# Optimization experiments

Measured on AMD Instinct MI355X. Metric: run time of the kernel, lower is better.

## Reference

```python
import jax, jax.numpy as jnp
import numpy as np

N_NODES = 50000
N_EDGES = 800000
N_GRAPHS = 128
INPUT_DIM = 64
HIDDEN = 64       # num_heads * dim_per_head = 4 * 16
N_HEADS = 4
DK = HIDDEN // N_HEADS   # 16, per-head key/query dim
DV = HIDDEN // N_HEADS   # 16, per-head value dim
NUM_LAYERS = 4           # -> 3 GIN layers
OUT_DIM = 16
LN_EPS = 1e-5


def layer_norm(x, g, b):
    mu = jnp.mean(x, axis=-1, keepdims=True)
    var = jnp.mean(jnp.square(x - mu), axis=-1, keepdims=True)
    return (x - mu) * jax.lax.rsqrt(var + LN_EPS) * g + b


def sab_block(x, Wq, Wk, Wv, Wo, ln_g, ln_b, add_residual):
    # x: [N, S, D_in]; pre-LN self-attention block (Set Transformer SAB)
    xin = layer_norm(x, ln_g, ln_b)
    q = jnp.einsum('nsd,dhk->nshk', xin, Wq)   # [N,S,H,dk]
    k = jnp.einsum('nsd,dhk->nshk', xin, Wk)
    v = jnp.einsum('nsd,dhk->nshk', xin, Wv)   # [N,S,H,dv]
    scores = jnp.einsum('nqhk,nshk->nhqs', q, k) / jnp.sqrt(jnp.asarray(DK, x.dtype))
    att = jax.nn.softmax(scores, axis=-1)
    o = jnp.einsum('nhqs,nshk->nqhk', att, v)
    o = o.reshape(o.shape[0], o.shape[1], N_HEADS * DV)
    o = o @ Wo                                  # [N,S,dim_out]
    if add_residual:
        o = o + x
    return o


def gin_aggregate(h, src, dst):
    # sum-neighbor aggregation; eps=0, learn_eps=False -> (1+0)*h + sum_nbrs
    msg = jax.ops.segment_sum(h[src], dst, num_segments=N_NODES)
    return h + msg


def setup_inputs() -> dict:
    key = jax.random.key(0)
    ks = jax.random.split(key, 16)
    s = 0.05
    feat = jax.random.normal(ks[0], (N_NODES, 4 * INPUT_DIM), dtype=jnp.float32)
    src = jax.random.randint(ks[1], (N_EDGES,), 0, N_NODES)
    dst = jax.random.randint(ks[2], (N_EDGES,), 0, N_NODES)
    graph_ids = jnp.sort(jax.random.randint(ks[3], (N_NODES,), 0, N_GRAPHS))
    L = NUM_LAYERS - 1  # 3 GIN layers, all same shapes (input_dim == hidden)
    Wq = jax.random.normal(ks[4], (L, HIDDEN, N_HEADS, DK), dtype=jnp.float32) * s
    Wk = jax.random.normal(ks[5], (L, HIDDEN, N_HEADS, DK), dtype=jnp.float32) * s
    Wv = jax.random.normal(ks[6], (L, HIDDEN, N_HEADS, DV), dtype=jnp.float32) * s
    Wo = jax.random.normal(ks[7], (L, N_HEADS * DV, HIDDEN), dtype=jnp.float32) * s
    sab_ln_g = jnp.ones((L, HIDDEN), dtype=jnp.float32)
    sab_ln_b = jnp.zeros((L, HIDDEN), dtype=jnp.float32)
    ln1_g = jnp.ones((L, HIDDEN), dtype=jnp.float32)
    ln1_b = jnp.zeros((L, HIDDEN), dtype=jnp.float32)
    ln2_g = jnp.ones((L, HIDDEN), dtype=jnp.float32)
    ln2_b = jnp.zeros((L, HIDDEN), dtype=jnp.float32)
    W_pred = jax.random.normal(ks[8], (NUM_LAYERS, HIDDEN, OUT_DIM), dtype=jnp.float32) * s
    b_pred = jnp.zeros((NUM_LAYERS, OUT_DIM), dtype=jnp.float32)
    return {"feat": feat, "src": src, "dst": dst, "graph_ids": graph_ids,
            "Wq": Wq, "Wk": Wk, "Wv": Wv, "Wo": Wo,
            "sab_ln_g": sab_ln_g, "sab_ln_b": sab_ln_b,
            "ln1_g": ln1_g, "ln1_b": ln1_b, "ln2_g": ln2_g, "ln2_b": ln2_b,
            "W_pred": W_pred, "b_pred": b_pred}


def reference(feat, src, dst, graph_ids, Wq, Wk, Wv, Wo,
              sab_ln_g, sab_ln_b, ln1_g, ln1_b, ln2_g, ln2_b, W_pred, b_pred):
    h = feat.reshape(N_NODES, -1, INPUT_DIM)   # [N, S, D]
    hidden_rep = [h]
    for i in range(NUM_LAYERS - 1):
        if i == 0:
            agg = gin_aggregate(h, src, dst)
            h = sab_block(agg, Wq[i], Wk[i], Wv[i], Wo[i],
                          sab_ln_g[i], sab_ln_b[i], add_residual=False)
        else:
            h_pre = layer_norm(h, ln1_g[i], ln1_b[i])
            agg = gin_aggregate(h_pre, src, dst)
            h = h + sab_block(agg, Wq[i], Wk[i], Wv[i], Wo[i],
                              sab_ln_g[i], sab_ln_b[i], add_residual=True)
        hidden_rep.append(layer_norm(jax.nn.relu(h), ln2_g[i], ln2_b[i]))
    score = jnp.zeros((N_GRAPHS, hidden_rep[0].shape[1], OUT_DIM), dtype=feat.dtype)
    for i, hh in enumerate(hidden_rep):
        pooled = jax.ops.segment_sum(hh, graph_ids, num_segments=N_GRAPHS)  # [B,S,D]
        score = score + pooled @ W_pred[i] + b_pred[i]
    return score
```

## Files before the change

### kernel.cpp

```cpp
#include <hip/hip_runtime.h>

#define NN 50000
#define NE 800000
#define NG 128
#define RREP 16
#define RSTRIDE 50048

typedef __attribute__((ext_vector_type(8))) short short8;
typedef __attribute__((ext_vector_type(4))) float f32x4;

__device__ __forceinline__ unsigned short f2bf(float f){
  union { float f; unsigned int u; } v; v.f = f;
  return (unsigned short)((v.u + 0x7fffu + ((v.u >> 16) & 1u)) >> 16);
}
__device__ __forceinline__ float bf2f(unsigned short h){
  union { unsigned int u; float f; } v; v.u = ((unsigned int)h) << 16;
  return v.f;
}

__global__ __launch_bounds__(256) void k_goff(const int* __restrict__ gid,
                                              int* __restrict__ goff){
  int i = blockIdx.x*256 + threadIdx.x;
  if (i >= NN) return;
  int c = gid[i];
  int p = (i == 0) ? -1 : gid[i-1];
  for (int g = p+1; g <= c; ++g) goff[g] = i;
  if (i == NN-1){
    for (int g = c+1; g <= NG; ++g) goff[g] = NN;
  }
}

__global__ __launch_bounds__(256) void k_count_rep(const int* __restrict__ idx,
                                                   int* __restrict__ cnt_rep, int n){
  int i = blockIdx.x*256 + threadIdx.x;
  int r = blockIdx.x & (RREP-1);
  if (i < n) atomicAdd(&cnt_rep[r*RSTRIDE + idx[i]], 1);
}

__global__ __launch_bounds__(256) void k_reduce_rep(const int* __restrict__ cnt_rep,
                                                    int* __restrict__ cnt){
  int i = blockIdx.x*256 + threadIdx.x;
  if (i < NN){
    int s = 0;
    #pragma unroll
    for (int r=0; r<RREP; ++r) s += cnt_rep[r*RSTRIDE + i];
    cnt[i] = s;
  }
}

__global__ __launch_bounds__(256) void k_blocksum(const int* __restrict__ in, int n,
                                                  int* __restrict__ bsum){
  __shared__ int ws4[4];
  int i = blockIdx.x*256 + threadIdx.x;
  int v = (i < n) ? in[i] : 0;
  #pragma unroll
  for (int d=1; d<64; d<<=1) v += __shfl_xor(v, d);
  int lane = threadIdx.x & 63, w = threadIdx.x >> 6;
  if (lane == 0) ws4[w] = v;
  __syncthreads();
  if (threadIdx.x == 0) bsum[blockIdx.x] = ws4[0]+ws4[1]+ws4[2]+ws4[3];
}

__global__ __launch_bounds__(256) void k_scan_small(const int* __restrict__ in, int n,
                                                    int* __restrict__ out){
  __shared__ int wsum[4];
  int tid = threadIdx.x, lane = tid & 63, w = tid >> 6;
  int v = (tid < n) ? in[tid] : 0;
  int x = v;
  #pragma unroll
  for (int d=1; d<64; d<<=1){ int y = __shfl_up(x, d); if (lane >= d) x += y; }
  if (lane == 63) wsum[w] = x;
  __syncthreads();
  int pre2 = 0;
  for (int j=0; j<w; ++j) pre2 += wsum[j];
  int incl = x + pre2;
  if (tid < n) out[tid] = incl - v;
  if (tid == n-1) out[n] = incl;
}

__global__ __launch_bounds__(256) void k_scan_apply(const int* __restrict__ in, int n,
                                                    const int* __restrict__ boff,
                                                    int* __restrict__ out){
  __shared__ int wsum[4];
  int tid = threadIdx.x, lane = tid & 63, w = tid >> 6;
  int i = blockIdx.x*256 + tid;
  int v = (i < n) ? in[i] : 0;
  int x = v;
  #pragma unroll
  for (int d=1; d<64; d<<=1){ int y = __shfl_up(x, d); if (lane >= d) x += y; }
  if (lane == 63) wsum[w] = x;
  __syncthreads();
  int pre2 = boff[blockIdx.x];
  for (int j=0; j<w; ++j) pre2 += wsum[j];
  int excl = x - v + pre2;
  if (i < n){
    out[i] = excl;
    if (i == n-1) out[n] = excl + v;
  }
}

__global__ __launch_bounds__(256) void k_fpos_rep(const int* __restrict__ cnt_rep,
                                                  const int* __restrict__ off,
                                                  int* __restrict__ fpos_rep){
  int i = blockIdx.x*256 + threadIdx.x;
  if (i < NN){
    int p = off[i];
    #pragma unroll
    for (int r=0; r<RREP; ++r){
      fpos_rep[r*RSTRIDE + i] = p;
      p += cnt_rep[r*RSTRIDE + i];
    }
  }
}

__global__ __launch_bounds__(256) void k_fill_rep(const int* __restrict__ src,
                                                  const int* __restrict__ dst,
                                                  int* __restrict__ fpos_rep,
                                                  int* __restrict__ csr, int n){
  int i = blockIdx.x*256 + threadIdx.x;
  int r = blockIdx.x & (RREP-1);
  if (i < n){
    int p = atomicAdd(&fpos_rep[r*RSTRIDE + dst[i]], 1);
    csr[p] = src[i];
  }
}

__global__ __launch_bounds__(256) void k_wt(const float* __restrict__ Wq,
                                            const float* __restrict__ Wk,
                                            const float* __restrict__ Wv,
                                            const float* __restrict__ Wo,
                                            unsigned short* __restrict__ Wt){
  int gid = blockIdx.x*256 + threadIdx.x;
  int l   = gid >> 14;
  int rem = gid & 16383;
  int mat = rem >> 12;
  int idx = rem & 4095;
  int c = idx >> 6, n = idx & 63;
  const float* srcp = (mat==0)?Wq:(mat==1)?Wk:(mat==2)?Wv:Wo;
  float v = srcp[l*4096 + idx];
  Wt[l*16384 + (mat*64 + n)*64 + c] = f2bf(v);
}

__global__ __launch_bounds__(256) void k_f2bf(const float* __restrict__ in,
                                              unsigned short* __restrict__ out){
  int i = blockIdx.x*256 + threadIdx.x;
  float4 v = ((const float4*)in)[i];
  ushort4 o; o.x=f2bf(v.x); o.y=f2bf(v.y); o.z=f2bf(v.z); o.w=f2bf(v.w);
  ((ushort4*)out)[i] = o;
}

__global__ __launch_bounds__(256) void k_aggregate(const unsigned short* __restrict__ pre,
                                                   const int* __restrict__ off,
                                                   const int* __restrict__ csr,
                                                   unsigned short* __restrict__ agg){
  int w = threadIdx.x >> 6, lane = threadIdx.x & 63;
  int node = blockIdx.x*4 + w;
  int s = off[node], e = off[node+1];
  const ushort4* base = (const ushort4*)pre;
  ushort4 u = base[node*64 + lane];
  float a0 = bf2f(u.x), a1 = bf2f(u.y), a2 = bf2f(u.z), a3 = bf2f(u.w);
  int i = s;
  for (; i + 4 <= e; i += 4){
    int n0 = csr[i], n1 = csr[i+1], n2 = csr[i+2], n3 = csr[i+3];
    ushort4 u0 = base[n0*64 + lane], u1 = base[n1*64 + lane];
    ushort4 u2 = base[n2*64 + lane], u3 = base[n3*64 + lane];
    a0 += bf2f(u0.x)+bf2f(u1.x)+bf2f(u2.x)+bf2f(u3.x);
    a1 += bf2f(u0.y)+bf2f(u1.y)+bf2f(u2.y)+bf2f(u3.y);
    a2 += bf2f(u0.z)+bf2f(u1.z)+bf2f(u2.z)+bf2f(u3.z);
    a3 += bf2f(u0.w)+bf2f(u1.w)+bf2f(u2.w)+bf2f(u3.w);
  }
  for (; i < e; ++i){
    int n0 = csr[i];
    ushort4 u0 = base[n0*64 + lane];
    a0 += bf2f(u0.x); a1 += bf2f(u0.y); a2 += bf2f(u0.z); a3 += bf2f(u0.w);
  }
  ushort4 o; o.x=f2bf(a0); o.y=f2bf(a1); o.z=f2bf(a2); o.w=f2bf(a3);
  ((ushort4*)agg)[node*64 + lane] = o;
}

__global__ __launch_bounds__(256) void k_sab(unsigned short* __restrict__ agg,
                                             unsigned short* __restrict__ h,
                                             unsigned short* __restrict__ pre_next,
                                             const unsigned short* __restrict__ Wt,
                                             const float* __restrict__ lng,
                                             const float* __restrict__ lnb,
                                             const float* __restrict__ g2,
                                             const float* __restrict__ b2,
                                             const float* __restrict__ g1,
                                             const float* __restrict__ b1,
                                             int residual, int write_pre, int write_h){
  __shared__ unsigned short xo_s[4][16][72];
  __shared__ unsigned short qkv_s[4][16][200];

  int tid = threadIdx.x;
  int w = tid >> 6, lane = tid & 63;
  int c16 = lane & 15, kb = lane >> 4;
  int R0 = blockIdx.x*64 + w*16;

  {
    float4 gv = ((const float4*)lng)[c16];
    float4 bv = ((const float4*)lnb)[c16];
    #pragma unroll
    for (int rr=0; rr<4; ++rr){
      int m = rr*4 + kb;
      ushort4 uv = ((const ushort4*)agg)[(R0+m)*16 + c16];
      float vx = bf2f(uv.x), vy = bf2f(uv.y), vz = bf2f(uv.z), vw = bf2f(uv.w);
      float s = vx+vy+vz+vw;
      float q = vx*vx+vy*vy+vz*vz+vw*vw;
      #pragma unroll
      for (int d=1; d<16; d<<=1){ s += __shfl_xor(s, d); q += __shfl_xor(q, d); }
      float mu = s*(1.f/64.f);
      float rs = rsqrtf(q*(1.f/64.f) - mu*mu + 1e-5f);
      ushort4 o;
      o.x=f2bf((vx-mu)*rs*gv.x+bv.x); o.y=f2bf((vy-mu)*rs*gv.y+bv.y);
      o.z=f2bf((vz-mu)*rs*gv.z+bv.z); o.w=f2bf((vw-mu)*rs*gv.w+bv.w);
      *(ushort4*)&xo_s[w][m][c16*4] = o;
    }
  }

  short8 a0 = *(const short8*)&xo_s[w][c16][kb*8];
  short8 a1 = *(const short8*)&xo_s[w][c16][32 + kb*8];
  f32x4 acc[12];
  #pragma unroll
  for (int t=0; t<12; ++t){
    short8 b0 = *(const short8*)&Wt[(t*16 + c16)*64 + kb*8];
    short8 b1 = *(const short8*)&Wt[(t*16 + c16)*64 + 32 + kb*8];
    f32x4 z = {0.f, 0.f, 0.f, 0.f};
    z = __builtin_amdgcn_mfma_f32_16x16x32_bf16(a0, b0, z, 0, 0, 0);
    z = __builtin_amdgcn_mfma_f32_16x16x32_bf16(a1, b1, z, 0, 0, 0);
    acc[t] = z;
  }
  #pragma unroll
  for (int t=0; t<12; ++t){
    #pragma unroll
    for (int r=0; r<4; ++r)
      qkv_s[w][kb*4 + r][t*16 + c16] = f2bf(acc[t][r]);
  }

  {
    int p = lane >> 2, qr = lane & 3;
    int ns = p >> 2, hd = p & 3;
    int mrow = ns*4 + qr;
    int qc = hd*16, kc = 64 + hd*16, vc = 128 + hd*16;
    float qv[16];
    short8 u0 = *(const short8*)&qkv_s[w][mrow][qc];
    short8 u1 = *(const short8*)&qkv_s[w][mrow][qc+8];
    #pragma unroll
    for (int j=0; j<8; ++j){
      qv[j]   = bf2f((unsigned short)u0[j]);
      qv[8+j] = bf2f((unsigned short)u1[j]);
    }
    float sc[4];
    #pragma unroll
    for (int kr=0; kr<4; ++kr){
      short8 k0 = *(const short8*)&qkv_s[w][ns*4+kr][kc];
      short8 k1 = *(const short8*)&qkv_s[w][ns*4+kr][kc+8];
      float d2 = 0.f;
      #pragma unroll
      for (int j=0; j<8; ++j){
        d2 += qv[j]  *bf2f((unsigned short)k0[j]);
        d2 += qv[8+j]*bf2f((unsigned short)k1[j]);
      }
      sc[kr] = d2 * 0.25f;
    }
    float mx = fmaxf(fmaxf(sc[0],sc[1]), fmaxf(sc[2],sc[3]));
    float e0=__expf(sc[0]-mx), e1=__expf(sc[1]-mx), e2=__expf(sc[2]-mx), e3=__expf(sc[3]-mx);
    float inv = 1.f/(e0+e1+e2+e3);
    float at[4] = {e0*inv, e1*inv, e2*inv, e3*inv};
    float ov[16];
    #pragma unroll
    for (int j=0; j<16; ++j) ov[j] = 0.f;
    #pragma unroll
    for (int kr=0; kr<4; ++kr){
      short8 v0 = *(const short8*)&qkv_s[w][ns*4+kr][vc];
      short8 v1 = *(const short8*)&qkv_s[w][ns*4+kr][vc+8];
      #pragma unroll
      for (int j=0; j<8; ++j){
        ov[j]   += at[kr]*bf2f((unsigned short)v0[j]);
        ov[8+j] += at[kr]*bf2f((unsigned short)v1[j]);
      }
    }
    short8 s0v, s1v;
    #pragma unroll
    for (int j=0; j<8; ++j){
      s0v[j] = (short)f2bf(ov[j]);
      s1v[j] = (short)f2bf(ov[8+j]);
    }
    *(short8*)&xo_s[w][mrow][qc]   = s0v;
    *(short8*)&xo_s[w][mrow][qc+8] = s1v;
  }

  short8 oa0 = *(const short8*)&xo_s[w][c16][kb*8];
  short8 oa1 = *(const short8*)&xo_s[w][c16][32 + kb*8];
  float val[4][4];
  #pragma unroll
  for (int t=0; t<4; ++t){
    short8 b0 = *(const short8*)&Wt[(192 + t*16 + c16)*64 + kb*8];
    short8 b1 = *(const short8*)&Wt[(192 + t*16 + c16)*64 + 32 + kb*8];
    f32x4 z = {0.f, 0.f, 0.f, 0.f};
    z = __builtin_amdgcn_mfma_f32_16x16x32_bf16(oa0, b0, z, 0, 0, 0);
    z = __builtin_amdgcn_mfma_f32_16x16x32_bf16(oa1, b1, z, 0, 0, 0);
    #pragma unroll
    for (int r=0; r<4; ++r){
      float v = z[r];
      if (residual){
        int gi = (R0 + kb*4 + r)*64 + t*16 + c16;
        v += bf2f(h[gi]) + bf2f(agg[gi]);
      }
      val[t][r] = v;
    }
  }

  float s1[4], q1[4], s2[4], q2[4];
  #pragma unroll
  for (int r=0; r<4; ++r){
    float a=0.f, b=0.f, c=0.f, d=0.f;
    #pragma unroll
    for (int t=0; t<4; ++t){
      float v = val[t][r];
      float rv = fmaxf(v, 0.f);
      a += v; b += v*v; c += rv; d += rv*rv;
    }
    s1[r]=a; q1[r]=b; s2[r]=c; q2[r]=d;
  }
  #pragma unroll
  for (int d=1; d<16; d<<=1){
    #pragma unroll
    for (int r=0; r<4; ++r){
      s1[r] += __shfl_xor(s1[r], d); q1[r] += __shfl_xor(q1[r], d);
      s2[r] += __shfl_xor(s2[r], d); q2[r] += __shfl_xor(q2[r], d);
    }
  }
  float mu1[4], rs1[4], mu2[4], rs2[4];
  #pragma unroll
  for (int r=0; r<4; ++r){
    mu1[r] = s1[r]*(1.f/64.f);
    rs1[r] = rsqrtf(q1[r]*(1.f/64.f) - mu1[r]*mu1[r] + 1e-5f);
    mu2[r] = s2[r]*(1.f/64.f);
    rs2[r] = rsqrtf(q2[r]*(1.f/64.f) - mu2[r]*mu2[r] + 1e-5f);
  }
  #pragma unroll
  for (int t=0; t<4; ++t){
    int col = t*16 + c16;
    float g2v = g2[col], b2v = b2[col];
    float g1v = 0.f, b1v = 0.f;
    if (write_pre){ g1v = g1[col]; b1v = b1[col]; }
    #pragma unroll
    for (int r=0; r<4; ++r){
      int gi = (R0 + kb*4 + r)*64 + col;
      float v = val[t][r];
      if (write_h) h[gi] = f2bf(v);
      float rv = fmaxf(v, 0.f);
      agg[gi] = f2bf((rv - mu2[r])*rs2[r]*g2v + b2v);
      if (write_pre)
        pre_next[gi] = f2bf((v - mu1[r])*rs1[r]*g1v + b1v);
    }
  }
}

__global__ __launch_bounds__(256) void k_pool8(const float* __restrict__ src,
                                               const int* __restrict__ goff,
                                               float* __restrict__ out){
  int g = blockIdx.x >> 3, sub = blockIdx.x & 7, t = threadIdx.x;
  int s = goff[g], e = goff[g+1], len = e - s;
  int s0 = s + ((len*sub) >> 3), e0 = s + ((len*(sub+1)) >> 3);
  float a0=0.f, a1=0.f;
  int n = s0;
  for (; n + 2 <= e0; n += 2){ a0 += src[n*256 + t]; a1 += src[(n+1)*256 + t]; }
  if (n < e0) a0 += src[n*256 + t];
  atomicAdd(&out[g*256 + t], a0 + a1);
}

__global__ __launch_bounds__(256) void k_pool8b(const unsigned short* __restrict__ src,
                                                const int* __restrict__ goff,
                                                float* __restrict__ out){
  int g = blockIdx.x >> 3, sub = blockIdx.x & 7, t = threadIdx.x;
  int s = goff[g], e = goff[g+1], len = e - s;
  int s0 = s + ((len*sub) >> 3), e0 = s + ((len*(sub+1)) >> 3);
  float a0=0.f, a1=0.f;
  int n = s0;
  for (; n + 2 <= e0; n += 2){ a0 += bf2f(src[n*256 + t]); a1 += bf2f(src[(n+1)*256 + t]); }
  if (n < e0) a0 += bf2f(src[n*256 + t]);
  atomicAdd(&out[g*256 + t], a0 + a1);
}

__global__ __launch_bounds__(256) void k_final(const float* __restrict__ pooled,
                                               const float* __restrict__ Wp,
                                               const float* __restrict__ bp,
                                               float* __restrict__ out){
  int t = blockIdx.x*256 + threadIdx.x;
  int b = t >> 6, s = (t >> 4) & 3, o = t & 15;
  float acc = 0.f;
  for (int i=0; i<4; ++i){
    acc += bp[i*16 + o];
    const float* pr = pooled + i*32768 + b*256 + s*64;
    const float* wp = Wp + i*1024 + o;
    float a = 0.f;
    #pragma unroll 8
    for (int c=0; c<64; ++c) a += pr[c]*wp[c*16];
    acc += a;
  }
  out[t] = acc;
}

static const size_t OFF_H    = 0;
static const size_t OFF_AGG  = 25600000;
static const size_t OFF_PRE  = 51200000;
static const size_t OFF_CSR  = 76800000;
static const size_t OFF_CNT  = 80000000;
static const size_t OFF_OFF  = 80200064;
static const size_t OFF_GOFF = 80400128;
static const size_t OFF_POOL = 80400704;
static const size_t OFF_WT   = 80924992;
static const size_t OFF_BSUM = 81023296;
static const size_t OFF_BOFF = 81024128;

extern "C" void kernel_launch(void* const* d_in, const int* in_sizes, int n_in,
                              void* d_out, int out_size, void* d_ws, size_t ws_size,
                              hipStream_t stream) {
  const float* feat = (const float*)d_in[0];
  const int*   src  = (const int*)d_in[1];
  const int*   dst  = (const int*)d_in[2];
  const int*   gid  = (const int*)d_in[3];
  const float* Wq   = (const float*)d_in[4];
  const float* Wk   = (const float*)d_in[5];
  const float* Wv   = (const float*)d_in[6];
  const float* Wo   = (const float*)d_in[7];
  const float* sg   = (const float*)d_in[8];
  const float* sb   = (const float*)d_in[9];
  const float* l1g  = (const float*)d_in[10];
  const float* l1b  = (const float*)d_in[11];
  const float* l2g  = (const float*)d_in[12];
  const float* l2b  = (const float*)d_in[13];
  const float* Wp   = (const float*)d_in[14];
  const float* bp   = (const float*)d_in[15];
  float* out = (float*)d_out;

  char* ws = (char*)d_ws;
  unsigned short* h      = (unsigned short*)(ws + OFF_H);
  unsigned short* agg    = (unsigned short*)(ws + OFF_AGG);
  unsigned short* pre    = (unsigned short*)(ws + OFF_PRE);
  int*            csr    = (int*)(ws + OFF_CSR);
  int*            cnt    = (int*)(ws + OFF_CNT);
  int*            off    = (int*)(ws + OFF_OFF);
  int*            goff   = (int*)(ws + OFF_GOFF);
  float*          pooled = (float*)(ws + OFF_POOL);
  unsigned short* Wt     = (unsigned short*)(ws + OFF_WT);
  int*            bsum   = (int*)(ws + OFF_BSUM);
  int*            boff   = (int*)(ws + OFF_BOFF);
  int*            cnt_rep  = (int*)(ws + OFF_H);
  int*            fpos_rep = (int*)(ws + OFF_H + (size_t)RREP*RSTRIDE*4);

  hipMemsetAsync(cnt_rep, 0, (size_t)RREP*RSTRIDE*4, stream);
  hipMemsetAsync(pooled, 0, 4*NG*256*sizeof(float), stream);

  k_count_rep<<<NE/256, 256, 0, stream>>>(dst, cnt_rep, NE);
  k_goff<<<(NN+255)/256, 256, 0, stream>>>(gid, goff);
  k_reduce_rep<<<(NN+255)/256, 256, 0, stream>>>(cnt_rep, cnt);
  k_blocksum<<<196, 256, 0, stream>>>(cnt, NN, bsum);
  k_scan_small<<<1, 256, 0, stream>>>(bsum, 196, boff);
  k_scan_apply<<<196, 256, 0, stream>>>(cnt, NN, boff, off);
  k_fpos_rep<<<(NN+255)/256, 256, 0, stream>>>(cnt_rep, off, fpos_rep);
  k_fill_rep<<<NE/256, 256, 0, stream>>>(src, dst, fpos_rep, csr, NE);

  k_wt<<<192, 256, 0, stream>>>(Wq, Wk, Wv, Wo, Wt);
  k_f2bf<<<12500, 256, 0, stream>>>(feat, pre);
  k_pool8<<<NG*8, 256, 0, stream>>>(feat, goff, pooled + 0*32768);

  k_aggregate<<<12500, 256, 0, stream>>>(pre, off, csr, agg);
  k_sab<<<3125, 256, 0, stream>>>(agg, h, pre, Wt + 0*16384,
                                  sg + 0, sb + 0, l2g + 0, l2b + 0,
                                  l1g + 1*64, l1b + 1*64, 0, 1, 1);
  k_pool8b<<<NG*8, 256, 0, stream>>>(agg, goff, pooled + 1*32768);

  for (int i = 1; i < 3; ++i){
    k_aggregate<<<12500, 256, 0, stream>>>(pre, off, csr, agg);
    int wp = (i < 2) ? 1 : 0;
    int wh = (i < 2) ? 1 : 0;
    k_sab<<<3125, 256, 0, stream>>>(agg, h, pre, Wt + i*16384,
                                    sg + i*64, sb + i*64, l2g + i*64, l2b + i*64,
                                    l1g + (i+1)*64, l1b + (i+1)*64, 1, wp, wh);
    k_pool8b<<<NG*8, 256, 0, stream>>>(agg, goff, pooled + (i+1)*32768);
  }

  k_final<<<32, 256, 0, stream>>>(pooled, Wp, bp, out);
}
```

Measured before the change: 670.4 us.

## Fuse neighbor aggregation into SAB layer kernel with ping-pong pre buffers

Measured after the change: 683.5 us. No clear change (+1.9%).

```diff
diff --git a/kernel.cpp b/kernel.cpp
--- a/kernel.cpp
+++ b/kernel.cpp
@@ -11,7 +11,7 @@
 
 __device__ __forceinline__ unsigned short f2bf(float f){
   union { float f; unsigned int u; } v; v.f = f;
-  return (unsigned short)((v.u + 0x7fffu + ((v.u >> 16) & 1u)) >> 16);
+  return (unsigned short)((v.u + 0x8000u) >> 16);
 }
 __device__ __forceinline__ float bf2f(unsigned short h){
   union { unsigned int u; float f; } v; v.u = ((unsigned int)h) << 16;
@@ -149,85 +149,81 @@
   ((ushort4*)out)[i] = o;
 }
 
-__global__ __launch_bounds__(256) void k_aggregate(const unsigned short* __restrict__ pre,
-                                                   const int* __restrict__ off,
-                                                   const int* __restrict__ csr,
-                                                   unsigned short* __restrict__ agg){
-  int w = threadIdx.x >> 6, lane = threadIdx.x & 63;
-  int node = blockIdx.x*4 + w;
-  int s = off[node], e = off[node+1];
-  const ushort4* base = (const ushort4*)pre;
-  ushort4 u = base[node*64 + lane];
-  float a0 = bf2f(u.x), a1 = bf2f(u.y), a2 = bf2f(u.z), a3 = bf2f(u.w);
-  int i = s;
-  for (; i + 4 <= e; i += 4){
-    int n0 = csr[i], n1 = csr[i+1], n2 = csr[i+2], n3 = csr[i+3];
-    ushort4 u0 = base[n0*64 + lane], u1 = base[n1*64 + lane];
-    ushort4 u2 = base[n2*64 + lane], u3 = base[n3*64 + lane];
-    a0 += bf2f(u0.x)+bf2f(u1.x)+bf2f(u2.x)+bf2f(u3.x);
-    a1 += bf2f(u0.y)+bf2f(u1.y)+bf2f(u2.y)+bf2f(u3.y);
-    a2 += bf2f(u0.z)+bf2f(u1.z)+bf2f(u2.z)+bf2f(u3.z);
-    a3 += bf2f(u0.w)+bf2f(u1.w)+bf2f(u2.w)+bf2f(u3.w);
-  }
-  for (; i < e; ++i){
-    int n0 = csr[i];
-    ushort4 u0 = base[n0*64 + lane];
-    a0 += bf2f(u0.x); a1 += bf2f(u0.y); a2 += bf2f(u0.z); a3 += bf2f(u0.w);
-  }
-  ushort4 o; o.x=f2bf(a0); o.y=f2bf(a1); o.z=f2bf(a2); o.w=f2bf(a3);
-  ((ushort4*)agg)[node*64 + lane] = o;
-}
-
-__global__ __launch_bounds__(256) void k_sab(unsigned short* __restrict__ agg,
-                                             unsigned short* __restrict__ h,
-                                             unsigned short* __restrict__ pre_next,
-                                             const unsigned short* __restrict__ Wt,
-                                             const float* __restrict__ lng,
-                                             const float* __restrict__ lnb,
-                                             const float* __restrict__ g2,
-                                             const float* __restrict__ b2,
-                                             const float* __restrict__ g1,
-                                             const float* __restrict__ b1,
-                                             int residual, int write_pre, int write_h){
+__global__ __launch_bounds__(256) void k_layer(const unsigned short* __restrict__ pre_in,
+                                               unsigned short* __restrict__ h,
+                                               unsigned short* __restrict__ lnout,
+                                               unsigned short* __restrict__ pre_next,
+                                               const int* __restrict__ off,
+                                               const int* __restrict__ csr,
+                                               const unsigned short* __restrict__ Wt,
+                                               const float* __restrict__ lng,
+                                               const float* __restrict__ lnb,
+                                               const float* __restrict__ g2,
+                                               const float* __restrict__ b2,
+                                               const float* __restrict__ g1,
+                                               const float* __restrict__ b1,
+                                               int residual, int write_pre, int write_h){
   __shared__ unsigned short xo_s[4][16][72];
+  __shared__ unsigned short agg_s[4][16][72];
   __shared__ unsigned short qkv_s[4][16][200];
 
   int tid = threadIdx.x;
   int w = tid >> 6, lane = tid & 63;
   int c16 = lane & 15, kb = lane >> 4;
   int R0 = blockIdx.x*64 + w*16;
-
-  {
-    float4 gv = ((const float4*)lng)[c16];
-    float4 bv = ((const float4*)lnb)[c16];
-    #pragma unroll
-    for (int rr=0; rr<4; ++rr){
-      int m = rr*4 + kb;
-      ushort4 uv = ((const ushort4*)agg)[(R0+m)*16 + c16];
-      float vx = bf2f(uv.x), vy = bf2f(uv.y), vz = bf2f(uv.z), vw = bf2f(uv.w);
-      float s = vx+vy+vz+vw;
-      float q = vx*vx+vy*vy+vz*vz+vw*vw;
-      #pragma unroll
-      for (int d=1; d<16; d<<=1){ s += __shfl_xor(s, d); q += __shfl_xor(q, d); }
-      float mu = s*(1.f/64.f);
-      float rs = rsqrtf(q*(1.f/64.f) - mu*mu + 1e-5f);
-      ushort4 o;
-      o.x=f2bf((vx-mu)*rs*gv.x+bv.x); o.y=f2bf((vy-mu)*rs*gv.y+bv.y);
-      o.z=f2bf((vz-mu)*rs*gv.z+bv.z); o.w=f2bf((vw-mu)*rs*gv.w+bv.w);
-      *(ushort4*)&xo_s[w][m][c16*4] = o;
-    }
-  }
-
-  short8 a0 = *(const short8*)&xo_s[w][c16][kb*8];
-  short8 a1 = *(const short8*)&xo_s[w][c16][32 + kb*8];
+  int node0 = blockIdx.x*16 + w*4;
+
+  const ushort4* base = (const ushort4*)pre_in;
+  float4 gv = ((const float4*)lng)[c16];
+  float4 bv = ((const float4*)lnb)[c16];
+
+  for (int nn=0; nn<4; ++nn){
+    int node = node0 + nn;
+    int s = off[node], e = off[node+1];
+    ushort4 u = base[node*64 + lane];
+    float a0 = bf2f(u.x), a1 = bf2f(u.y), a2 = bf2f(u.z), a3 = bf2f(u.w);
+    int i = s;
+    for (; i + 4 <= e; i += 4){
+      int n0 = csr[i], n1 = csr[i+1], n2 = csr[i+2], n3 = csr[i+3];
+      ushort4 u0 = base[n0*64 + lane], u1 = base[n1*64 + lane];
+      ushort4 u2 = base[n2*64 + lane], u3 = base[n3*64 + lane];
+      a0 += bf2f(u0.x)+bf2f(u1.x)+bf2f(u2.x)+bf2f(u3.x);
+      a1 += bf2f(u0.y)+bf2f(u1.y)+bf2f(u2.y)+bf2f(u3.y);
+      a2 += bf2f(u0.z)+bf2f(u1.z)+bf2f(u2.z)+bf2f(u3.z);
+      a3 += bf2f(u0.w)+bf2f(u1.w)+bf2f(u2.w)+bf2f(u3.w);
+    }
+    for (; i < e; ++i){
+      int n0 = csr[i];
+      ushort4 u0 = base[n0*64 + lane];
+      a0 += bf2f(u0.x); a1 += bf2f(u0.y); a2 += bf2f(u0.z); a3 += bf2f(u0.w);
+    }
+    int m = nn*4 + kb;
+    if (residual){
+      ushort4 o; o.x=f2bf(a0); o.y=f2bf(a1); o.z=f2bf(a2); o.w=f2bf(a3);
+      *(ushort4*)&agg_s[w][m][c16*4] = o;
+    }
+    float s0 = a0+a1+a2+a3;
+    float q0 = a0*a0+a1*a1+a2*a2+a3*a3;
+    #pragma unroll
+    for (int d=1; d<16; d<<=1){ s0 += __shfl_xor(s0, d); q0 += __shfl_xor(q0, d); }
+    float mu = s0*(1.f/64.f);
+    float rs = rsqrtf(q0*(1.f/64.f) - mu*mu + 1e-5f);
+    ushort4 o;
+    o.x=f2bf((a0-mu)*rs*gv.x+bv.x); o.y=f2bf((a1-mu)*rs*gv.y+bv.y);
+    o.z=f2bf((a2-mu)*rs*gv.z+bv.z); o.w=f2bf((a3-mu)*rs*gv.w+bv.w);
+    *(ushort4*)&xo_s[w][m][c16*4] = o;
+  }
+
+  short8 a0v = *(const short8*)&xo_s[w][c16][kb*8];
+  short8 a1v = *(const short8*)&xo_s[w][c16][32 + kb*8];
   f32x4 acc[12];
   #pragma unroll
   for (int t=0; t<12; ++t){
     short8 b0 = *(const short8*)&Wt[(t*16 + c16)*64 + kb*8];
     short8 b1 = *(const short8*)&Wt[(t*16 + c16)*64 + 32 + kb*8];
     f32x4 z = {0.f, 0.f, 0.f, 0.f};
-    z = __builtin_amdgcn_mfma_f32_16x16x32_bf16(a0, b0, z, 0, 0, 0);
-    z = __builtin_amdgcn_mfma_f32_16x16x32_bf16(a1, b1, z, 0, 0, 0);
+    z = __builtin_amdgcn_mfma_f32_16x16x32_bf16(a0v, b0, z, 0, 0, 0);
+    z = __builtin_amdgcn_mfma_f32_16x16x32_bf16(a1v, b1, z, 0, 0, 0);
     acc[t] = z;
   }
   #pragma unroll
@@ -290,70 +286,65 @@
     *(short8*)&xo_s[w][mrow][qc+8] = s1v;
   }
 
-  short8 oa0 = *(const short8*)&xo_s[w][c16][kb*8];
-  short8 oa1 = *(const short8*)&xo_s[w][c16][32 + kb*8];
-  float val[4][4];
-  #pragma unroll
-  for (int t=0; t<4; ++t){
-    short8 b0 = *(const short8*)&Wt[(192 + t*16 + c16)*64 + kb*8];
-    short8 b1 = *(const short8*)&Wt[(192 + t*16 + c16)*64 + 32 + kb*8];
-    f32x4 z = {0.f, 0.f, 0.f, 0.f};
-    z = __builtin_amdgcn_mfma_f32_16x16x32_bf16(oa0, b0, z, 0, 0, 0);
-    z = __builtin_amdgcn_mfma_f32_16x16x32_bf16(oa1, b1, z, 0, 0, 0);
-    #pragma unroll
-    for (int r=0; r<4; ++r){
-      float v = z[r];
-      if (residual){
-        int gi = (R0 + kb*4 + r)*64 + t*16 + c16;
-        v += bf2f(h[gi]) + bf2f(agg[gi]);
-      }
-      val[t][r] = v;
-    }
-  }
-
-  float s1[4], q1[4], s2[4], q2[4];
-  #pragma unroll
-  for (int r=0; r<4; ++r){
-    float a=0.f, b=0.f, c=0.f, d=0.f;
+  {
+    short8 oa0 = *(const short8*)&xo_s[w][c16][kb*8];
+    short8 oa1 = *(const short8*)&xo_s[w][c16][32 + kb*8];
     #pragma unroll
     for (int t=0; t<4; ++t){
-      float v = val[t][r];
-      float rv = fmaxf(v, 0.f);
-      a += v; b += v*v; c += rv; d += rv*rv;
-    }
-    s1[r]=a; q1[r]=b; s2[r]=c; q2[r]=d;
-  }
-  #pragma unroll
-  for (int d=1; d<16; d<<=1){
-    #pragma unroll
-    for (int r=0; r<4; ++r){
-      s1[r] += __shfl_xor(s1[r], d); q1[r] += __shfl_xor(q1[r], d);
-      s2[r] += __shfl_xor(s2[r], d); q2[r] += __shfl_xor(q2[r], d);
-    }
-  }
-  float mu1[4], rs1[4], mu2[4], rs2[4];
-  #pragma unroll
-  for (int r=0; r<4; ++r){
-    mu1[r] = s1[r]*(1.f/64.f);
-    rs1[r] = rsqrtf(q1[r]*(1.f/64.f) - mu1[r]*mu1[r] + 1e-5f);
-    mu2[r] = s2[r]*(1.f/64.f);
-    rs2[r] = rsqrtf(q2[r]*(1.f/64.f) - mu2[r]*mu2[r] + 1e-5f);
-  }
-  #pragma unroll
-  for (int t=0; t<4; ++t){
-    int col = t*16 + c16;
-    float g2v = g2[col], b2v = b2[col];
-    float g1v = 0.f, b1v = 0.f;
-    if (write_pre){ g1v = g1[col]; b1v = b1[col]; }
-    #pragma unroll
-    for (int r=0; r<4; ++r){
-      int gi = (R0 + kb*4 + r)*64 + col;
-      float v = val[t][r];
-      if (write_h) h[gi] = f2bf(v);
-      float rv = fmaxf(v, 0.f);
-      agg[gi] = f2bf((rv - mu2[r])*rs2[r]*g2v + b2v);
-      if (write_pre)
-        pre_next[gi] = f2bf((v - mu1[r])*rs1[r]*g1v + b1v);
+      short8 b0 = *(const short8*)&Wt[(192 + t*16 + c16)*64 + kb*8];
+      short8 b1 = *(const short8*)&Wt[(192 + t*16 + c16)*64 + 32 + kb*8];
+      f32x4 z = {0.f, 0.f, 0.f, 0.f};
+      z = __builtin_amdgcn_mfma_f32_16x16x32_bf16(oa0, b0, z, 0, 0, 0);
+      z = __builtin_amdgcn_mfma_f32_16x16x32_bf16(oa1, b1, z, 0, 0, 0);
+      #pragma unroll
+      for (int r=0; r<4; ++r)
+        xo_s[w][kb*4 + r][t*16 + c16] = f2bf(z[r]);
+    }
+  }
+
+  float4 g2v = ((const float4*)g2)[c16];
+  float4 b2v = ((const float4*)b2)[c16];
+  float4 g1v, b1v;
+  if (write_pre){ g1v = ((const float4*)g1)[c16]; b1v = ((const float4*)b1)[c16]; }
+  #pragma unroll
+  for (int rr=0; rr<4; ++rr){
+    int m = rr*4 + kb;
+    int row = R0 + m;
+    ushort4 uv = *(const ushort4*)&xo_s[w][m][c16*4];
+    float v0 = bf2f(uv.x), v1 = bf2f(uv.y), v2 = bf2f(uv.z), v3 = bf2f(uv.w);
+    if (residual){
+      ushort4 hh = ((const ushort4*)h)[row*16 + c16];
+      ushort4 ag = *(const ushort4*)&agg_s[w][m][c16*4];
+      v0 += bf2f(hh.x) + bf2f(ag.x);
+      v1 += bf2f(hh.y) + bf2f(ag.y);
+      v2 += bf2f(hh.z) + bf2f(ag.z);
+      v3 += bf2f(hh.w) + bf2f(ag.w);
+    }
+    float r0 = fmaxf(v0,0.f), r1 = fmaxf(v1,0.f), r2 = fmaxf(v2,0.f), r3 = fmaxf(v3,0.f);
+    float s1 = v0+v1+v2+v3, q1 = v0*v0+v1*v1+v2*v2+v3*v3;
+    float s2 = r0+r1+r2+r3, q2 = r0*r0+r1*r1+r2*r2+r3*r3;
+    #pragma unroll
+    for (int d=1; d<16; d<<=1){
+      s1 += __shfl_xor(s1, d); q1 += __shfl_xor(q1, d);
+      s2 += __shfl_xor(s2, d); q2 += __shfl_xor(q2, d);
+    }
+    float mu1 = s1*(1.f/64.f), rs1 = rsqrtf(q1*(1.f/64.f) - mu1*mu1 + 1e-5f);
+    float mu2 = s2*(1.f/64.f), rs2 = rsqrtf(q2*(1.f/64.f) - mu2*mu2 + 1e-5f);
+    if (write_h){
+      ushort4 o; o.x=f2bf(v0); o.y=f2bf(v1); o.z=f2bf(v2); o.w=f2bf(v3);
+      ((ushort4*)h)[row*16 + c16] = o;
+    }
+    {
+      ushort4 o;
+      o.x=f2bf((r0-mu2)*rs2*g2v.x+b2v.x); o.y=f2bf((r1-mu2)*rs2*g2v.y+b2v.y);
+      o.z=f2bf((r2-mu2)*rs2*g2v.z+b2v.z); o.w=f2bf((r3-mu2)*rs2*g2v.w+b2v.w);
+      ((ushort4*)lnout)[row*16 + c16] = o;
+    }
+    if (write_pre){
+      ushort4 o;
+      o.x=f2bf((v0-mu1)*rs1*g1v.x+b1v.x); o.y=f2bf((v1-mu1)*rs1*g1v.y+b1v.y);
+      o.z=f2bf((v2-mu1)*rs1*g1v.z+b1v.z); o.w=f2bf((v3-mu1)*rs1*g1v.w+b1v.w);
+      ((ushort4*)pre_next)[row*16 + c16] = o;
     }
   }
 }
@@ -403,17 +394,18 @@
   out[t] = acc;
 }
 
-static const size_t OFF_H    = 0;
-static const size_t OFF_AGG  = 25600000;
-static const size_t OFF_PRE  = 51200000;
-static const size_t OFF_CSR  = 76800000;
-static const size_t OFF_CNT  = 80000000;
-static const size_t OFF_OFF  = 80200064;
-static const size_t OFF_GOFF = 80400128;
-static const size_t OFF_POOL = 80400704;
-static const size_t OFF_WT   = 80924992;
-static const size_t OFF_BSUM = 81023296;
-static const size_t OFF_BOFF = 81024128;
+static const size_t OFF_H     = 0;
+static const size_t OFF_LNOUT = 25600000;
+static const size_t OFF_PRE0  = 51200000;
+static const size_t OFF_PRE1  = 76800000;
+static const size_t OFF_CSR   = 102400000;
+static const size_t OFF_CNT   = 105600000;
+static const size_t OFF_OFF   = 105800064;
+static const size_t OFF_GOFF  = 106000128;
+static const size_t OFF_POOL  = 106000704;
+static const size_t OFF_WT    = 106525056;
+static const size_t OFF_BSUM  = 106623360;
+static const size_t OFF_BOFF  = 106624192;
 
 extern "C" void kernel_launch(void* const* d_in, const int* in_sizes, int n_in,
                               void* d_out, int out_size, void* d_ws, size_t ws_size,
@@ -438,8 +430,9 @@
 
   char* ws = (char*)d_ws;
   unsigned short* h      = (unsigned short*)(ws + OFF_H);
-  unsigned short* agg    = (unsigned short*)(ws + OFF_AGG);
-  unsigned short* pre    = (unsigned short*)(ws + OFF_PRE);
+  unsigned short* lnout  = (unsigned short*)(ws + OFF_LNOUT);
+  unsigned short* pre0   = (unsigned short*)(ws + OFF_PRE0);
+  unsigned short* pre1   = (unsigned short*)(ws + OFF_PRE1);
   int*            csr    = (int*)(ws + OFF_CSR);
   int*            cnt    = (int*)(ws + OFF_CNT);
   int*            off    = (int*)(ws + OFF_OFF);
@@ -464,24 +457,23 @@
   k_fill_rep<<<NE/256, 256, 0, stream>>>(src, dst, fpos_rep, csr, NE);
 
   k_wt<<<192, 256, 0, stream>>>(Wq, Wk, Wv, Wo, Wt);
-  k_f2bf<<<12500, 256, 0, stream>>>(feat, pre);
+  k_f2bf<<<12500, 256, 0, stream>>>(feat, pre0);
   k_pool8<<<NG*8, 256, 0, stream>>>(feat, goff, pooled + 0*32768);
 
-  k_aggregate<<<12500, 256, 0, stream>>>(pre, off, csr, agg);
-  k_sab<<<3125, 256, 0, stream>>>(agg, h, pre, Wt + 0*16384,
-                                  sg + 0, sb + 0, l2g + 0, l2b + 0,
-                                  l1g + 1*64, l1b + 1*64, 0, 1, 1);
-  k_pool8b<<<NG*8, 256, 0, stream>>>(agg, goff, pooled + 1*32768);
-
-  for (int i = 1; i < 3; ++i){
-    k_aggregate<<<12500, 256, 0, stream>>>(pre, off, csr, agg);
-    int wp = (i < 2) ? 1 : 0;
-    int wh = (i < 2) ? 1 : 0;
-    k_sab<<<3125, 256, 0, stream>>>(agg, h, pre, Wt + i*16384,
-                                    sg + i*64, sb + i*64, l2g + i*64, l2b + i*64,
-                                    l1g + (i+1)*64, l1b + (i+1)*64, 1, wp, wh);
-    k_pool8b<<<NG*8, 256, 0, stream>>>(agg, goff, pooled + (i+1)*32768);
-  }
+  k_layer<<<3125, 256, 0, stream>>>(pre0, h, lnout, pre1, off, csr, Wt + 0*16384,
+                                    sg + 0, sb + 0, l2g + 0, l2b + 0,
+                                    l1g + 1*64, l1b + 1*64, 0, 1, 1);
+  k_pool8b<<<NG*8, 256, 0, stream>>>(lnout, goff, pooled + 1*32768);
+
+  k_layer<<<3125, 256, 0, stream>>>(pre1, h, lnout, pre0, off, csr, Wt + 1*16384,
+                                    sg + 1*64, sb + 1*64, l2g + 1*64, l2b + 1*64,
+                                    l1g + 2*64, l1b + 2*64, 1, 1, 1);
+  k_pool8b<<<NG*8, 256, 0, stream>>>(lnout, goff, pooled + 2*32768);
+
+  k_layer<<<3125, 256, 0, stream>>>(pre0, h, lnout, pre1, off, csr, Wt + 2*16384,
+                                    sg + 2*64, sb + 2*64, l2g + 2*64, l2b + 2*64,
+                                    l1g + 2*64, l1b + 2*64, 1, 0, 0);
+  k_pool8b<<<NG*8, 256, 0, stream>>>(lnout, goff, pooled + 3*32768);
 
   k_final<<<32, 256, 0, stream>>>(pooled, Wp, bp, out);
 }
```
